# Optimization experiments

Measured on AMD Instinct MI355X. Metric: run time of the kernel, lower is better.

## Reference

```python
import jax, jax.numpy as jnp
import numpy as np

# SuperposedExpert: K parallel TT-factorized FFN paths + holographic routing.
# d_model=1024 factorized as [32,32]; d_ff=4096 as [64,64]; tt_ranks=[1,16,1] (r0/r2 squeezed).
K, D_MODEL, D_FF, RANK = 4, 1024, 4096, 16
IN1, IN2 = 32, 32          # factorize_for_tt(d_model)
F1, F2 = 64, 64            # factorize_for_tt(d_ff)
TEMP = 1.0                 # routing_temperature


def setup_inputs() -> dict:
    key = jax.random.key(0)
    ks = jax.random.split(key, 8)
    s = 0.05
    tokens = jax.random.normal(ks[0], (2048, D_MODEL), dtype=jnp.float32)
    # TT cores for ffn1: d_model -> d_ff  (input_dims [32,32], output_dims [64,64])
    ffn1_core1 = jax.random.normal(ks[1], (K, IN1, F1, RANK), dtype=jnp.float32) * s
    ffn1_core2 = jax.random.normal(ks[2], (K, RANK, IN2, F2), dtype=jnp.float32) * s
    # TT cores for ffn2: d_ff -> d_model (input_dims [64,64], output_dims [32,32])
    ffn2_core1 = jax.random.normal(ks[3], (K, F1, IN1, RANK), dtype=jnp.float32) * s
    ffn2_core2 = jax.random.normal(ks[4], (K, RANK, F2, IN2), dtype=jnp.float32) * s
    # Holographic routing params (hd_dim == d_model -> identity HD projection)
    pb = jax.random.normal(ks[5], (K, D_MODEL), dtype=jnp.float32)
    path_bases = pb / jnp.linalg.norm(pb, axis=-1, keepdims=True)  # orthogonal-ish init
    path_weights = jax.random.normal(ks[6], (K, D_MODEL), dtype=jnp.float32) * s
    return {
        'tokens': tokens,
        'ffn1_core1': ffn1_core1, 'ffn1_core2': ffn1_core2,
        'ffn2_core1': ffn2_core1, 'ffn2_core2': ffn2_core2,
        'path_bases': path_bases, 'path_weights': path_weights,
    }


def reference(tokens, ffn1_core1, ffn1_core2, ffn2_core1, ffn2_core2,
              path_bases, path_weights):
    N = tokens.shape[0]
    # ---- K superposed TT-FFN paths ----
    x3 = tokens.reshape(N, IN1, IN2)  # [n, a, b]
    # TT matmul 1: y[x,y] = sum_{a,b,r} G1[a,x,r] G2[r,b,y] x[a,b]
    h = jnp.einsum('nab,kaxr,krby->knxy', x3, ffn1_core1, ffn1_core2)
    h = jax.nn.gelu(h.reshape(K, N, D_FF))  # quantum_activation stand-in
    h3 = h.reshape(K, N, F1, F2)
    y = jnp.einsum('knab,kaxr,krby->knxy', h3, ffn2_core1, ffn2_core2)
    y = y.reshape(K, N, D_MODEL)  # per-path outputs
    # ---- Holographic HD routing (hd_dim == d_model: identity projection) ----
    logits = jnp.einsum('nd,kd->nk', tokens, path_bases) / TEMP
    gates = jax.nn.softmax(logits, axis=-1)  # [n, k]
    # Collapse superposition: per-path elementwise HD modulation + gated sum
    out = jnp.einsum('knd,kd,nk->nd', y, 1.0 + path_weights, gates)
    return out
```

## Files before the change

kernel.cpp:

```cpp
#include <hip/hip_runtime.h>
#include <stdint.h>

#define GAS __attribute__((address_space(1)))
#define LAS __attribute__((address_space(3)))

typedef __attribute__((ext_vector_type(8))) short short8;
typedef __attribute__((ext_vector_type(16))) float f32x16;

static constexpr int N_TOK = 2048;
static constexpr int DM    = 1024;
static constexpr int DF    = 4096;
static constexpr int KP    = 4;

__device__ inline unsigned short f2bf(float f) {
  union { float f; uint32_t u; } v; v.f = f;
  uint32_t u = v.u;
  u += 0x7FFFu + ((u >> 16) & 1u);
  return (unsigned short)(u >> 16);
}

__device__ inline uint32_t pk_bf(float lo, float hi) {
  union { float f; uint32_t u; } a, b; a.f = lo; b.f = hi;
  uint32_t ul = a.u + 0x7FFFu + ((a.u >> 16) & 1u);
  uint32_t uh = b.u + 0x7FFFu + ((b.u >> 16) & 1u);
  return (ul >> 16) | (uh & 0xFFFF0000u);
}

__device__ inline float gelu_gate(float v, float g) {
  float t0 = v * v;
  float u  = v * __builtin_fmaf(t0, -0.10294456f, -2.3022539f);
  float e  = __builtin_amdgcn_exp2f(u);
  float r  = __builtin_amdgcn_rcpf(1.0f + e);
  return v * g * r;
}

__device__ inline void gld16(const void* g, void* l) {
  __builtin_amdgcn_global_load_lds((const GAS void*)g, (LAS void*)l, 16, 0, 0);
}

__global__ __launch_bounds__(256) void setup_kernel(
    const float* __restrict__ tokens, const float* __restrict__ pb,
    const float* __restrict__ c11, const float* __restrict__ c12,
    const float* __restrict__ c21, const float* __restrict__ c22,
    float* __restrict__ gates, unsigned short* __restrict__ xb,
    unsigned short* __restrict__ w1t, unsigned short* __restrict__ w2t) {
  __shared__ float sh[2048];
  const int blk = blockIdx.x;
  const int t = threadIdx.x;
  if (blk < 16384) {
    const int k = blk >> 12, f = blk & 4095;
    const int x = f >> 6, y = f & 63;
    float* s1 = sh;
    float* s2 = sh + 512;
    for (int i = t; i < 512; i += 256) {
      int a = i >> 4, r = i & 15;
      s1[i] = c11[(((size_t)(k * 32 + a)) * 64 + x) * 16 + r];
    }
    for (int i = t; i < 512; i += 256) {
      int r = i >> 5, b = i & 31;
      s2[i] = c12[(((size_t)(k * 16 + r)) * 32 + b) * 64 + y];
    }
    __syncthreads();
    unsigned short* wrow = w1t + ((size_t)k * DF + f) * DM;
    const int d0 = t * 4;
    const int a = d0 >> 5, b0 = d0 & 31;
    float s[4] = {0.f, 0.f, 0.f, 0.f};
#pragma unroll
    for (int r = 0; r < 16; ++r) {
      float cv = s1[a * 16 + r];
#pragma unroll
      for (int j = 0; j < 4; ++j) s[j] = __builtin_fmaf(cv, s2[r * 32 + b0 + j], s[j]);
    }
    ushort4 o; o.x = f2bf(s[0]); o.y = f2bf(s[1]); o.z = f2bf(s[2]); o.w = f2bf(s[3]);
    *(ushort4*)(wrow + d0) = o;
  } else if (blk < 20480) {
    const int kd = blk - 16384;
    const int k = kd >> 10, d = kd & 1023;
    const int x = d >> 5, y = d & 31;
    float* s1 = sh;
    float* s2 = sh + 1024;
    for (int i = t; i < 1024; i += 256) {
      int a = i >> 4, r = i & 15;
      s1[i] = c21[(((size_t)(k * 64 + a)) * 32 + x) * 16 + r];
    }
    for (int i = t; i < 1024; i += 256) {
      int r = i >> 6, b = i & 63;
      s2[i] = c22[(((size_t)(k * 16 + r)) * 64 + b) * 32 + y];
    }
    __syncthreads();
    unsigned short* wrow = w2t + ((size_t)k * DM + d) * DF;
#pragma unroll
    for (int jj = 0; jj < 4; ++jj) {
      int f4 = t * 16 + jj * 4;
      int a = f4 >> 6, b0 = f4 & 63;
      float s[4] = {0.f, 0.f, 0.f, 0.f};
#pragma unroll
      for (int r = 0; r < 16; ++r) {
        float cv = s1[a * 16 + r];
#pragma unroll
        for (int j = 0; j < 4; ++j) s[j] = __builtin_fmaf(cv, s2[r * 64 + b0 + j], s[j]);
      }
      ushort4 o; o.x = f2bf(s[0]); o.y = f2bf(s[1]); o.z = f2bf(s[2]); o.w = f2bf(s[3]);
      *(ushort4*)(wrow + f4) = o;
    }
  } else {
    const int wave = t >> 6, lane = t & 63;
    const int n = (blk - 20480) * 4 + wave;
    float s0 = 0.f, s1v = 0.f, s2v = 0.f, s3v = 0.f;
    const float4* tr = (const float4*)(tokens + (size_t)n * DM);
#pragma unroll
    for (int j = 0; j < 4; ++j) {
      int idx = j * 64 + lane;
      float4 tv = tr[idx];
      ushort4 b;
      b.x = f2bf(tv.x); b.y = f2bf(tv.y); b.z = f2bf(tv.z); b.w = f2bf(tv.w);
      *(ushort4*)(xb + (size_t)n * DM + idx * 4) = b;
      float4 q;
      q = ((const float4*)(pb + 0 * DM))[idx]; s0  += tv.x*q.x + tv.y*q.y + tv.z*q.z + tv.w*q.w;
      q = ((const float4*)(pb + 1 * DM))[idx]; s1v += tv.x*q.x + tv.y*q.y + tv.z*q.z + tv.w*q.w;
      q = ((const float4*)(pb + 2 * DM))[idx]; s2v += tv.x*q.x + tv.y*q.y + tv.z*q.z + tv.w*q.w;
      q = ((const float4*)(pb + 3 * DM))[idx]; s3v += tv.x*q.x + tv.y*q.y + tv.z*q.z + tv.w*q.w;
    }
#pragma unroll
    for (int off = 32; off > 0; off >>= 1) {
      s0  += __shfl_xor(s0, off);
      s1v += __shfl_xor(s1v, off);
      s2v += __shfl_xor(s2v, off);
      s3v += __shfl_xor(s3v, off);
    }
    if (lane == 0) {
      float m = fmaxf(fmaxf(s0, s1v), fmaxf(s2v, s3v));
      float e0 = __expf(s0 - m), e1 = __expf(s1v - m), e2 = __expf(s2v - m), e3 = __expf(s3v - m);
      float inv = 1.0f / (e0 + e1 + e2 + e3);
      float4 g; g.x = e0 * inv; g.y = e1 * inv; g.z = e2 * inv; g.w = e3 * inv;
      *(float4*)(gates + n * 4) = g;
    }
  }
}

__global__ __launch_bounds__(256) void gemm1(
    const unsigned short* __restrict__ xb, const unsigned short* __restrict__ w1t,
    const float* __restrict__ gates, unsigned short* __restrict__ hg) {
  __shared__ __align__(16) unsigned short As[128 * 64];
  __shared__ __align__(16) unsigned short Bs[128 * 64];
  const int t = threadIdx.x, lane = t & 63, wv = t >> 6;
  const int m0 = blockIdx.x * 128;
  const int f0 = blockIdx.y * 128;
  const int kp = blockIdx.z;
  const unsigned short* B = w1t + (size_t)kp * DF * DM;
  f32x16 acc[2][2] = {};
  const int srow = t >> 3;
  const int sbase = ((t & 7) ^ (srow & 7) ^ (srow >> 3)) * 8;
  const int wfrow = (wv >> 1) * 64, wtcol = (wv & 1) * 64;
  const int l31 = lane & 31, khalf = lane >> 5;
  const int rsw = (l31 & 7) ^ (l31 >> 3);
  char* AsB = (char*)As;
  char* BsB = (char*)Bs;
  for (int k0 = 0; k0 < DM; k0 += 64) {
#pragma unroll
    for (int i = 0; i < 4; ++i) {
      int row = i * 32 + srow;
      int sc = sbase ^ ((i & 1) * 32);
      gld16(xb + (size_t)(m0 + row) * DM + k0 + sc, AsB + i * 4096 + t * 16);
      gld16(B + (size_t)(f0 + row) * DM + k0 + sc, BsB + i * 4096 + t * 16);
    }
    __syncthreads();
#pragma unroll
    for (int s = 0; s < 4; ++s) {
      const int lc = s * 2 + khalf;
      short8 a[2], b[2];
#pragma unroll
      for (int mi = 0; mi < 2; ++mi) {
        const int pc = ((lc ^ rsw ^ (mi * 4)) & 7) * 8;
        a[mi] = *(const short8*)(Bs + (wfrow + mi * 32 + l31) * 64 + pc);
      }
#pragma unroll
      for (int ni = 0; ni < 2; ++ni) {
        const int pc = ((lc ^ rsw ^ (ni * 4)) & 7) * 8;
        b[ni] = *(const short8*)(As + (wtcol + ni * 32 + l31) * 64 + pc);
      }
#pragma unroll
      for (int mi = 0; mi < 2; ++mi)
#pragma unroll
        for (int ni = 0; ni < 2; ++ni)
          acc[mi][ni] = __builtin_amdgcn_mfma_f32_32x32x16_bf16(a[mi], b[ni], acc[mi][ni], 0, 0, 0);
    }
    __syncthreads();
  }
  unsigned short* H = hg + (size_t)kp * N_TOK * DF;
  const int rbase = 4 * khalf;
#pragma unroll
  for (int ni = 0; ni < 2; ++ni) {
    int n_g = m0 + wtcol + ni * 32 + l31;
    float g = gates[n_g * 4 + kp];
    unsigned short* hrow = H + (size_t)n_g * DF + f0;
#pragma unroll
    for (int mi = 0; mi < 2; ++mi) {
      int fbase = wfrow + mi * 32 + rbase;
#pragma unroll
      for (int gq = 0; gq < 4; ++gq) {
        float r0 = gelu_gate(acc[mi][ni][4 * gq + 0], g);
        float r1 = gelu_gate(acc[mi][ni][4 * gq + 1], g);
        float r2 = gelu_gate(acc[mi][ni][4 * gq + 2], g);
        float r3 = gelu_gate(acc[mi][ni][4 * gq + 3], g);
        uint2 p; p.x = pk_bf(r0, r1); p.y = pk_bf(r2, r3);
        *(uint2*)(hrow + fbase + 8 * gq) = p;
      }
    }
  }
}

__global__ __launch_bounds__(256) void gemm2(
    const unsigned short* __restrict__ hg, const unsigned short* __restrict__ w2t,
    const float* __restrict__ pw, float* __restrict__ part) {
  __shared__ __align__(16) unsigned short As[128 * 64];
  __shared__ __align__(16) unsigned short Bs[128 * 64];
  const int t = threadIdx.x, lane = t & 63, wv = t >> 6;
  const int m0 = blockIdx.x * 128;
  const int n0 = blockIdx.y * 128;
  const int kp = blockIdx.z;
  const unsigned short* A = hg + (size_t)kp * N_TOK * DF;
  const unsigned short* B = w2t + (size_t)kp * DM * DF;
  f32x16 acc[2][2] = {};
  const int srow = t >> 3;
  const int sbase = ((t & 7) ^ (srow & 7) ^ (srow >> 3)) * 8;
  const int wdrow = (wv >> 1) * 64, wtcol = (wv & 1) * 64;
  const int l31 = lane & 31, khalf = lane >> 5;
  const int rsw = (l31 & 7) ^ (l31 >> 3);
  char* AsB = (char*)As;
  char* BsB = (char*)Bs;
  for (int k0 = 0; k0 < DF; k0 += 64) {
#pragma unroll
    for (int i = 0; i < 4; ++i) {
      int row = i * 32 + srow;
      int sc = sbase ^ ((i & 1) * 32);
      gld16(A + (size_t)(m0 + row) * DF + k0 + sc, AsB + i * 4096 + t * 16);
      gld16(B + (size_t)(n0 + row) * DF + k0 + sc, BsB + i * 4096 + t * 16);
    }
    __syncthreads();
#pragma unroll
    for (int s = 0; s < 4; ++s) {
      const int lc = s * 2 + khalf;
      short8 a[2], b[2];
#pragma unroll
      for (int mi = 0; mi < 2; ++mi) {
        const int pc = ((lc ^ rsw ^ (mi * 4)) & 7) * 8;
        a[mi] = *(const short8*)(Bs + (wdrow + mi * 32 + l31) * 64 + pc);
      }
#pragma unroll
      for (int ni = 0; ni < 2; ++ni) {
        const int pc = ((lc ^ rsw ^ (ni * 4)) & 7) * 8;
        b[ni] = *(const short8*)(As + (wtcol + ni * 32 + l31) * 64 + pc);
      }
#pragma unroll
      for (int mi = 0; mi < 2; ++mi)
#pragma unroll
        for (int ni = 0; ni < 2; ++ni)
          acc[mi][ni] = __builtin_amdgcn_mfma_f32_32x32x16_bf16(a[mi], b[ni], acc[mi][ni], 0, 0, 0);
    }
    __syncthreads();
  }
  float* P = part + (size_t)kp * N_TOK * DM;
  const int rbase = 4 * khalf;
  float4 pwv[2][4];
#pragma unroll
  for (int mi = 0; mi < 2; ++mi)
#pragma unroll
    for (int gq = 0; gq < 4; ++gq) {
      float4 w = *(const float4*)(pw + kp * DM + n0 + wdrow + mi * 32 + rbase + 8 * gq);
      pwv[mi][gq].x = 1.0f + w.x; pwv[mi][gq].y = 1.0f + w.y;
      pwv[mi][gq].z = 1.0f + w.z; pwv[mi][gq].w = 1.0f + w.w;
    }
#pragma unroll
  for (int ni = 0; ni < 2; ++ni) {
    int tok = m0 + wtcol + ni * 32 + l31;
    float* prow = P + (size_t)tok * DM + n0;
#pragma unroll
    for (int mi = 0; mi < 2; ++mi) {
      int dbase = wdrow + mi * 32 + rbase;
#pragma unroll
      for (int gq = 0; gq < 4; ++gq) {
        float4 o;
        o.x = pwv[mi][gq].x * acc[mi][ni][4 * gq + 0];
        o.y = pwv[mi][gq].y * acc[mi][ni][4 * gq + 1];
        o.z = pwv[mi][gq].z * acc[mi][ni][4 * gq + 2];
        o.w = pwv[mi][gq].w * acc[mi][ni][4 * gq + 3];
        *(float4*)(prow + dbase + 8 * gq) = o;
      }
    }
  }
}

__global__ __launch_bounds__(256) void reduce_k(
    const float* __restrict__ part, float* __restrict__ out) {
  const size_t i = ((size_t)blockIdx.x * 256 + threadIdx.x) * 4;
  const size_t S = (size_t)N_TOK * DM;
  float4 a = *(const float4*)(part + i);
  float4 b = *(const float4*)(part + S + i);
  float4 c = *(const float4*)(part + 2 * S + i);
  float4 d = *(const float4*)(part + 3 * S + i);
  float4 r;
  r.x = a.x + b.x + c.x + d.x;
  r.y = a.y + b.y + c.y + d.y;
  r.z = a.z + b.z + c.z + d.z;
  r.w = a.w + b.w + c.w + d.w;
  *(float4*)(out + i) = r;
}

extern "C" void kernel_launch(void* const* d_in, const int* in_sizes, int n_in,
                              void* d_out, int out_size, void* d_ws, size_t ws_size,
                              hipStream_t stream) {
  const float* tokens = (const float*)d_in[0];
  const float* f1c1   = (const float*)d_in[1];
  const float* f1c2   = (const float*)d_in[2];
  const float* f2c1   = (const float*)d_in[3];
  const float* f2c2   = (const float*)d_in[4];
  const float* pb     = (const float*)d_in[5];
  const float* pw     = (const float*)d_in[6];
  float* out = (float*)d_out;

  char* ws = (char*)d_ws;
  unsigned short* xb  = (unsigned short*)(ws);
  unsigned short* w1t = (unsigned short*)(ws + (4ull  << 20));
  float*          part = (float*)(ws + (4ull << 20));
  unsigned short* w2t = (unsigned short*)(ws + (36ull << 20));
  unsigned short* hg  = (unsigned short*)(ws + (68ull << 20));
  float*          gates = (float*)(ws + (132ull << 20));

  hipLaunchKernelGGL(setup_kernel, dim3(20992), dim3(256), 0, stream,
                     tokens, pb, f1c1, f1c2, f2c1, f2c2, gates, xb, w1t, w2t);
  hipLaunchKernelGGL(gemm1, dim3(16, 32, KP), dim3(256), 0, stream, xb, w1t, gates, hg);
  hipLaunchKernelGGL(gemm2, dim3(16, 8, KP), dim3(256), 0, stream, hg, w2t, pw, part);
  hipLaunchKernelGGL(reduce_k, dim3(2048), dim3(256), 0, stream, part, out);
}
```

Measured before the change: 298.3 us.

## Tile TT weight materialization so each block builds many rows with register reuse

The setup kernel that expands the TT cores into dense bf16 weight matrices now has each block produce 16 output rows instead of one. Core slices are loaded once per block with float4 loads into padded shared memory, and each thread accumulates several output vectors in registers. The grid shrinks from about 21k blocks to 1792. This removes redundant core reloads and per-block overhead, at the cost of much more shared memory per block (about 70KB) and higher register pressure, which lowers occupancy.

```diff
diff --git a/kernel.cpp b/kernel.cpp
--- a/kernel.cpp
+++ b/kernel.cpp
@@ -44,68 +44,129 @@
     const float* __restrict__ c21, const float* __restrict__ c22,
     float* __restrict__ gates, unsigned short* __restrict__ xb,
     unsigned short* __restrict__ w1t, unsigned short* __restrict__ w2t) {
-  __shared__ float sh[2048];
+  __shared__ __align__(16) float sh[17568];
   const int blk = blockIdx.x;
   const int t = threadIdx.x;
-  if (blk < 16384) {
-    const int k = blk >> 12, f = blk & 4095;
-    const int x = f >> 6, y = f & 63;
+  if (blk < 1024) {
+    const int k = blk >> 8, x = (blk >> 2) & 63, y0 = (blk & 3) * 16;
     float* s1 = sh;
     float* s2 = sh + 512;
-    for (int i = t; i < 512; i += 256) {
-      int a = i >> 4, r = i & 15;
-      s1[i] = c11[(((size_t)(k * 32 + a)) * 64 + x) * 16 + r];
-    }
-    for (int i = t; i < 512; i += 256) {
-      int r = i >> 5, b = i & 31;
-      s2[i] = c12[(((size_t)(k * 16 + r)) * 32 + b) * 64 + y];
-    }
-    __syncthreads();
-    unsigned short* wrow = w1t + ((size_t)k * DF + f) * DM;
-    const int d0 = t * 4;
-    const int a = d0 >> 5, b0 = d0 & 31;
-    float s[4] = {0.f, 0.f, 0.f, 0.f};
+    if (t < 128) {
+      int a = t >> 2, rq = (t & 3) * 4;
+      *(float4*)(s1 + a * 16 + rq) =
+          *(const float4*)(c11 + (((size_t)(k * 32 + a)) * 64 + x) * 16 + rq);
+    }
+#pragma unroll
+    for (int j = 0; j < 8; ++j) {
+      int i = t + j * 256;
+      int rb = i >> 2, yy = (i & 3) * 4;
+      int r = rb >> 5, b = rb & 31;
+      float4 v = *(const float4*)(c12 + (((size_t)(k * 16 + r)) * 32 + b) * 64 + y0 + yy);
+      s2[(yy + 0) * 522 + rb] = v.x;
+      s2[(yy + 1) * 522 + rb] = v.y;
+      s2[(yy + 2) * 522 + rb] = v.z;
+      s2[(yy + 3) * 522 + rb] = v.w;
+    }
+    __syncthreads();
+    const int y = y0 + (t >> 4);
+    const int col = t & 15;
+    const int a0 = col * 2;
+    const float* s2y = s2 + (t >> 4) * 522;
+    float4 a0q[4], a1q[4];
+#pragma unroll
+    for (int q = 0; q < 4; ++q) {
+      a0q[q] = *(const float4*)(s1 + a0 * 16 + q * 4);
+      a1q[q] = *(const float4*)(s1 + (a0 + 1) * 16 + q * 4);
+    }
+    const float* a0s = (const float*)a0q;
+    const float* a1s = (const float*)a1q;
+    float4 acc0[8] = {}, acc1[8] = {};
 #pragma unroll
     for (int r = 0; r < 16; ++r) {
-      float cv = s1[a * 16 + r];
-#pragma unroll
-      for (int j = 0; j < 4; ++j) s[j] = __builtin_fmaf(cv, s2[r * 32 + b0 + j], s[j]);
-    }
-    ushort4 o; o.x = f2bf(s[0]); o.y = f2bf(s[1]); o.z = f2bf(s[2]); o.w = f2bf(s[3]);
-    *(ushort4*)(wrow + d0) = o;
-  } else if (blk < 20480) {
-    const int kd = blk - 16384;
-    const int k = kd >> 10, d = kd & 1023;
-    const int x = d >> 5, y = d & 31;
+      float cv0 = a0s[r], cv1 = a1s[r];
+      const float* row = s2y + r * 32;
+#pragma unroll
+      for (int q = 0; q < 8; ++q) {
+        float4 v = *(const float4*)(row + q * 4);
+        acc0[q].x = __builtin_fmaf(cv0, v.x, acc0[q].x);
+        acc0[q].y = __builtin_fmaf(cv0, v.y, acc0[q].y);
+        acc0[q].z = __builtin_fmaf(cv0, v.z, acc0[q].z);
+        acc0[q].w = __builtin_fmaf(cv0, v.w, acc0[q].w);
+        acc1[q].x = __builtin_fmaf(cv1, v.x, acc1[q].x);
+        acc1[q].y = __builtin_fmaf(cv1, v.y, acc1[q].y);
+        acc1[q].z = __builtin_fmaf(cv1, v.z, acc1[q].z);
+        acc1[q].w = __builtin_fmaf(cv1, v.w, acc1[q].w);
+      }
+    }
+    unsigned short* wrow = w1t + ((size_t)k * DF + x * 64 + y) * DM + col * 64;
+#pragma unroll
+    for (int q = 0; q < 8; ++q) {
+      ushort4 o0, o1;
+      o0.x = f2bf(acc0[q].x); o0.y = f2bf(acc0[q].y);
+      o0.z = f2bf(acc0[q].z); o0.w = f2bf(acc0[q].w);
+      o1.x = f2bf(acc1[q].x); o1.y = f2bf(acc1[q].y);
+      o1.z = f2bf(acc1[q].z); o1.w = f2bf(acc1[q].w);
+      *(ushort4*)(wrow + q * 4) = o0;
+      *(ushort4*)(wrow + 32 + q * 4) = o1;
+    }
+  } else if (blk < 1280) {
+    const int bb = blk - 1024;
+    const int k = bb >> 6, x = (bb >> 1) & 31, y0 = (bb & 1) * 16;
     float* s1 = sh;
     float* s2 = sh + 1024;
-    for (int i = t; i < 1024; i += 256) {
-      int a = i >> 4, r = i & 15;
-      s1[i] = c21[(((size_t)(k * 64 + a)) * 32 + x) * 16 + r];
-    }
-    for (int i = t; i < 1024; i += 256) {
-      int r = i >> 6, b = i & 63;
-      s2[i] = c22[(((size_t)(k * 16 + r)) * 64 + b) * 32 + y];
-    }
-    __syncthreads();
-    unsigned short* wrow = w2t + ((size_t)k * DM + d) * DF;
-#pragma unroll
-    for (int jj = 0; jj < 4; ++jj) {
-      int f4 = t * 16 + jj * 4;
-      int a = f4 >> 6, b0 = f4 & 63;
-      float s[4] = {0.f, 0.f, 0.f, 0.f};
+    {
+      int a = t >> 2, rq = (t & 3) * 4;
+      *(float4*)(s1 + a * 16 + rq) =
+          *(const float4*)(c21 + (((size_t)(k * 64 + a)) * 32 + x) * 16 + rq);
+    }
+#pragma unroll
+    for (int j = 0; j < 16; ++j) {
+      int i = t + j * 256;
+      int rb = i >> 2, yy = (i & 3) * 4;
+      int r = rb >> 6, b = rb & 63;
+      float4 v = *(const float4*)(c22 + (((size_t)(k * 16 + r)) * 64 + b) * 32 + y0 + yy);
+      s2[(yy + 0) * 1034 + rb] = v.x;
+      s2[(yy + 1) * 1034 + rb] = v.y;
+      s2[(yy + 2) * 1034 + rb] = v.z;
+      s2[(yy + 3) * 1034 + rb] = v.w;
+    }
+    __syncthreads();
+    const int y = y0 + (t >> 4);
+    const int col = t & 15;
+    const float* s2y = s2 + (t >> 4) * 1034;
+    unsigned short* wrow = w2t + ((size_t)k * DM + x * 32 + y) * DF;
+#pragma unroll
+    for (int p = 0; p < 4; ++p) {
+      int a = col * 4 + p;
+      float4 aq[4];
+#pragma unroll
+      for (int q = 0; q < 4; ++q) aq[q] = *(const float4*)(s1 + a * 16 + q * 4);
+      const float* as_ = (const float*)aq;
+      float4 acc[16] = {};
 #pragma unroll
       for (int r = 0; r < 16; ++r) {
-        float cv = s1[a * 16 + r];
-#pragma unroll
-        for (int j = 0; j < 4; ++j) s[j] = __builtin_fmaf(cv, s2[r * 64 + b0 + j], s[j]);
-      }
-      ushort4 o; o.x = f2bf(s[0]); o.y = f2bf(s[1]); o.z = f2bf(s[2]); o.w = f2bf(s[3]);
-      *(ushort4*)(wrow + f4) = o;
+        float cv = as_[r];
+        const float* row = s2y + r * 64;
+#pragma unroll
+        for (int q = 0; q < 16; ++q) {
+          float4 v = *(const float4*)(row + q * 4);
+          acc[q].x = __builtin_fmaf(cv, v.x, acc[q].x);
+          acc[q].y = __builtin_fmaf(cv, v.y, acc[q].y);
+          acc[q].z = __builtin_fmaf(cv, v.z, acc[q].z);
+          acc[q].w = __builtin_fmaf(cv, v.w, acc[q].w);
+        }
+      }
+#pragma unroll
+      for (int q = 0; q < 16; ++q) {
+        ushort4 o;
+        o.x = f2bf(acc[q].x); o.y = f2bf(acc[q].y);
+        o.z = f2bf(acc[q].z); o.w = f2bf(acc[q].w);
+        *(ushort4*)(wrow + a * 64 + q * 4) = o;
+      }
     }
   } else {
     const int wave = t >> 6, lane = t & 63;
-    const int n = (blk - 20480) * 4 + wave;
+    const int n = (blk - 1280) * 4 + wave;
     float s0 = 0.f, s1v = 0.f, s2v = 0.f, s3v = 0.f;
     const float4* tr = (const float4*)(tokens + (size_t)n * DM);
 #pragma unroll
@@ -327,7 +388,7 @@
   unsigned short* hg  = (unsigned short*)(ws + (68ull << 20));
   float*          gates = (float*)(ws + (132ull << 20));
 
-  hipLaunchKernelGGL(setup_kernel, dim3(20992), dim3(256), 0, stream,
+  hipLaunchKernelGGL(setup_kernel, dim3(1792), dim3(256), 0, stream,
                      tokens, pb, f1c1, f1c2, f2c1, f2c2, gates, xb, w1t, w2t);
   hipLaunchKernelGGL(gemm1, dim3(16, 32, KP), dim3(256), 0, stream, xb, w1t, gates, hg);
   hipLaunchKernelGGL(gemm2, dim3(16, 8, KP), dim3(256), 0, stream, hg, w2t, pw, part);
```

Result: slower. 628.1 us (+110.5%).
